# Optimization experiments

Hardware: AMD Instinct MI355X
Metric: run time of the kernel (lower is better)

The kernel has to match this reference:

```python
import jax, jax.numpy as jnp
import numpy as np

NUM_CATS = 8
ACTION_DIM = 64
HIDDEN = 1024  # out_type.size == config.hidden_size
N_TOKENS = 4096  # B*T
N_BATCH = 128    # timesteps batch; tiled to N_TOKENS in forward


def sinusoidal_pos_encoding(t, dim):
    # standard transformer sinusoidal encoding; t: (N,) -> (N, dim)
    half = dim // 2
    div = jnp.exp(jnp.arange(half, dtype=jnp.float32) * (-np.log(10000.0) / half))
    ang = t.astype(jnp.float32)[:, None] * div[None, :]          # (N, half)
    pe = jnp.stack([jnp.sin(ang), jnp.cos(ang)], axis=-1)        # (N, half, 2)
    return pe.reshape(t.shape[0], dim)


def cat_linear(x, W, b, cat_ids):
    """Per-category linear (gather -> per-group GEMM -> scatter-back, fused).
    x: (N, din), W: (C, din, dout), b: (C, dout), cat_ids: (N,) int.
    Mathematically identical to the torch loop over unique cat ids."""
    y_all = jnp.einsum('nd,cdo->nco', x, W)                      # dense dispatch over C
    y = jnp.take_along_axis(y_all, cat_ids[:, None, None], axis=1)[:, 0, :]
    return y + b[cat_ids]


def setup_inputs() -> dict:
    key = jax.random.key(0)
    ks = jax.random.split(key, 9)
    inp = {
        'actions': jax.random.normal(ks[0], (N_TOKENS, ACTION_DIM), dtype=jnp.float32),
        'timesteps': jax.random.randint(ks[1], (N_BATCH,), 0, 1000, dtype=jnp.int32),
        'cat_ids': jax.random.randint(ks[2], (N_TOKENS,), 0, NUM_CATS, dtype=jnp.int32),
        'W1': jax.random.normal(ks[3], (NUM_CATS, ACTION_DIM, HIDDEN), dtype=jnp.float32) / np.sqrt(ACTION_DIM),
        'b1': jax.random.normal(ks[4], (NUM_CATS, HIDDEN), dtype=jnp.float32) * 0.02,
        'W2': jax.random.normal(ks[5], (NUM_CATS, 2 * HIDDEN, HIDDEN), dtype=jnp.float32) / np.sqrt(2 * HIDDEN),
        'b2': jax.random.normal(ks[6], (NUM_CATS, HIDDEN), dtype=jnp.float32) * 0.02,
        'W3': jax.random.normal(ks[7], (NUM_CATS, HIDDEN, HIDDEN), dtype=jnp.float32) / np.sqrt(HIDDEN),
        'b3': jax.random.normal(ks[8], (NUM_CATS, HIDDEN), dtype=jnp.float32) * 0.02,
    }
    return inp


def reference(actions, timesteps, cat_ids, W1, b1, W2, b2, W3, b3):
    n = actions.shape[0]
    # timesteps.repeat(B // timesteps.shape[0]) in torch tiles the whole tensor
    t_full = jnp.tile(timesteps, n // timesteps.shape[0])        # (N,)
    a_emb = cat_linear(actions, W1, b1, cat_ids)                 # (N, H)
    tau_emb = sinusoidal_pos_encoding(t_full, HIDDEN).astype(a_emb.dtype)
    x = jnp.concatenate([a_emb, tau_emb], axis=-1)               # (N, 2H)
    x = jax.nn.silu(cat_linear(x, W2, b2, cat_ids))              # swish
    x = cat_linear(x, W3, b3, cat_ids)                           # (N, H)
    return x
```

## Files before the change

kernel.cpp:

```cpp
#include <hip/hip_runtime.h>
#include <cmath>


#define NTOK 4096
#define HID  1024
#define NC   8
#define MPAD 4224

typedef _Float16 f16;
typedef _Float16 f16x8 __attribute__((ext_vector_type(8)));
typedef float    f32x4 __attribute__((ext_vector_type(4)));

#define GLDS16(g, l) __builtin_amdgcn_global_load_lds(                      \
    (const __attribute__((address_space(1))) void*)(g),                     \
    (__attribute__((address_space(3))) void*)(l), 16, 0, 0)

__global__ void build_perm_kernel(const int* __restrict__ cat,
                                  int* __restrict__ perm,
                                  int* __restrict__ cat_off) {
  __shared__ int cnt[NC];
  __shared__ int off[NC + 1];
  const int tid = threadIdx.x;
  if (tid < NC) cnt[tid] = 0;
  __syncthreads();
  for (int n = tid; n < NTOK; n += blockDim.x) atomicAdd(&cnt[cat[n]], 1);
  __syncthreads();
  if (tid == 0) {
    int s = 0;
    for (int c = 0; c < NC; ++c) { off[c] = s; s += cnt[c]; }
    off[NC] = s;
  }
  __syncthreads();
  if (tid < NC) cnt[tid] = off[tid];
  if (tid <= NC) cat_off[tid] = off[tid];
  __syncthreads();
  for (int n = tid; n < NTOK; n += blockDim.x) {
    int pos = atomicAdd(&cnt[cat[n]], 1);
    perm[pos] = n;
  }
}

__global__ void tau16_kernel(const int* __restrict__ ts, f16* __restrict__ tau) {
  const int b = blockIdx.x;
  const float t = (float)ts[b];
  const float cdiv = -0.017988946039015984f;
  for (int i = threadIdx.x; i < HID / 2; i += blockDim.x) {
    float ang = t * expf(cdiv * (float)i);
    tau[(size_t)b * HID + 2 * i]     = (f16)sinf(ang);
    tau[(size_t)b * HID + 2 * i + 1] = (f16)cosf(ang);
  }
}

__global__ void gather_kernel(const float* __restrict__ actions,
                              const f16* __restrict__ tau,
                              const int* __restrict__ perm,
                              f16* __restrict__ act_g, f16* __restrict__ xcat) {
  const int r = blockIdx.x;
  const int tok = perm[r];
  const int t = threadIdx.x;
  if (t < 64) act_g[(size_t)r * 64 + t] = (f16)actions[(size_t)tok * 64 + t];
  const uint4* src = (const uint4*)(tau + (size_t)(tok & 127) * HID);
  uint4* dst = (uint4*)(xcat + (size_t)r * 2048 + HID);
  dst[t] = src[t];
}

__global__ __launch_bounds__(256) void wcvt_kernel(const float* __restrict__ W,
                                                   f16* __restrict__ Wt, int K) {
  const int c = blockIdx.z, k0 = blockIdx.y * 64, n0 = blockIdx.x * 64;
  __shared__ f16 tl[64][68];
  const int tid = threadIdx.x;
  const int rr = tid >> 4, cs = (tid & 15) * 4;
  const float* src = W + ((size_t)c * K + k0) * HID + n0;
#pragma unroll
  for (int it = 0; it < 4; ++it) {
    const int kr = rr + it * 16;
    float4 v = *(const float4*)(src + (size_t)kr * HID + cs);
    tl[kr][cs + 0] = (f16)v.x;
    tl[kr][cs + 1] = (f16)v.y;
    tl[kr][cs + 2] = (f16)v.z;
    tl[kr][cs + 3] = (f16)v.w;
  }
  __syncthreads();
  f16* dst = Wt + ((size_t)c * HID + n0) * K + k0;
#pragma unroll
  for (int it = 0; it < 4; ++it) {
    const int nr = rr + it * 16;
    union { f16 h[4]; uint2 u; } pk;
    pk.h[0] = tl[cs + 0][nr];
    pk.h[1] = tl[cs + 1][nr];
    pk.h[2] = tl[cs + 2][nr];
    pk.h[3] = tl[cs + 3][nr];
    *(uint2*)(dst + (size_t)nr * K + cs) = pk.u;
  }
}

template <int K, int MODE>
__global__ __launch_bounds__(512) void mfma_gemm(
    const f16* __restrict__ A, const f16* __restrict__ Wt,
    const float* __restrict__ Bias, const int* __restrict__ perm,
    const int* __restrict__ cat_off, void* __restrict__ OutV) {
  constexpr int PA = (MODE == 0) ? 64 : (MODE == 1) ? 2048 : 1024;
  constexpr int NT = K / 32;
  const int c = blockIdx.z;
  const int g0 = cat_off[c], cnt = cat_off[c + 1] - g0;
  const int m0 = blockIdx.y * 128;
  if (m0 >= cnt) return;
  const int n0 = blockIdx.x * 128;

  __shared__ f16 As[2][4096];
  __shared__ f16 Bs[2][4096];
  __shared__ int rows[128];

  const int tid = threadIdx.x;
  const int lane = tid & 63, wid = tid >> 6;

  if (MODE == 2 && tid < 128) {
    int m = m0 + tid;
    if (m > cnt - 1) m = cnt - 1;
    rows[tid] = perm[g0 + m];
  }

  const f16* Abase = A + (size_t)(g0 + m0) * PA;
  const f16* Bbase = Wt + ((size_t)c * HID + n0) * K;
  const int srow = tid >> 2, sks = (tid & 3) * 8;

  f32x4 acc[2][4];
#pragma unroll
  for (int i = 0; i < 2; ++i)
#pragma unroll
    for (int j = 0; j < 4; ++j) acc[i][j] = (f32x4){0.f, 0.f, 0.f, 0.f};

  const int wm = wid >> 1, wn = wid & 1;
  const int fr = lane & 15, fk = (lane >> 4) * 8;

#define STAGE(buf, kt)                                                \
  do {                                                                \
    GLDS16(Abase + (size_t)srow * PA + (kt) + sks, &As[buf][tid * 8]); \
    GLDS16(Bbase + (size_t)srow * K + (kt) + sks, &Bs[buf][tid * 8]);  \
  } while (0)

  STAGE(0, 0);
  __syncthreads();
  int cur = 0;
  for (int t = 0; t < NT; ++t) {
    if (t + 1 < NT) STAGE(cur ^ 1, (t + 1) * 32);
    f16x8 a[2], b[4];
#pragma unroll
    for (int i = 0; i < 2; ++i)
      a[i] = *(const f16x8*)&As[cur][(wm * 32 + i * 16 + fr) * 32 + fk];
#pragma unroll
    for (int j = 0; j < 4; ++j)
      b[j] = *(const f16x8*)&Bs[cur][(wn * 64 + j * 16 + fr) * 32 + fk];
#pragma unroll
    for (int i = 0; i < 2; ++i)
#pragma unroll
      for (int j = 0; j < 4; ++j)
        acc[i][j] = __builtin_amdgcn_mfma_f32_16x16x32_f16(a[i], b[j], acc[i][j], 0, 0, 0);
    __syncthreads();
    cur ^= 1;
  }
#undef STAGE

#pragma unroll
  for (int i = 0; i < 2; ++i) {
    const int mlbase = wm * 32 + i * 16 + (lane >> 4) * 4;
#pragma unroll
    for (int j = 0; j < 4; ++j) {
      const int col = wn * 64 + j * 16 + fr;
      const float bb = Bias[c * HID + n0 + col];
#pragma unroll
      for (int q = 0; q < 4; ++q) {
        const int ml = mlbase + q;
        if (m0 + ml >= cnt) continue;
        float v = acc[i][j][q] + bb;
        if (MODE == 1) v = v / (1.0f + __expf(-v));
        if (MODE == 2) {
          ((float*)OutV)[(size_t)rows[ml] * HID + n0 + col] = v;
        } else if (MODE == 1) {
          ((f16*)OutV)[(size_t)(g0 + m0 + ml) * HID + n0 + col] = (f16)v;
        } else {
          ((f16*)OutV)[(size_t)(g0 + m0 + ml) * 2048 + n0 + col] = (f16)v;
        }
      }
    }
  }
}

extern "C" void kernel_launch(void* const* d_in, const int* in_sizes, int n_in,
                              void* d_out, int out_size, void* d_ws, size_t ws_size,
                              hipStream_t stream) {
  const float* actions   = (const float*)d_in[0];
  const int*   timesteps = (const int*)d_in[1];
  const int*   cat_ids   = (const int*)d_in[2];
  const float* W1 = (const float*)d_in[3];
  const float* b1 = (const float*)d_in[4];
  const float* W2 = (const float*)d_in[5];
  const float* b2 = (const float*)d_in[6];
  const float* W3 = (const float*)d_in[7];
  const float* b3 = (const float*)d_in[8];
  float* out = (float*)d_out;

  char* ws = (char*)d_ws;
  const size_t MiB = 1u << 20;
  int* perm    = (int*)(ws + 0);
  int* cat_off = (int*)(ws + (16u << 10));
  f16* tau16   = (f16*)(ws + (32u << 10));
  f16* act_g   = (f16*)(ws + (512u << 10));
  f16* Wt1     = (f16*)(ws + 2 * MiB);
  f16* xcat    = (f16*)(ws + 3 * MiB);
  f16* h       = (f16*)(ws + 20 * MiB);
  f16* Wt2     = (f16*)(ws + 29 * MiB);
  f16* Wt3     = (f16*)(ws + 61 * MiB);

  build_perm_kernel<<<1, 256, 0, stream>>>(cat_ids, perm, cat_off);
  tau16_kernel<<<128, 256, 0, stream>>>(timesteps, tau16);
  gather_kernel<<<NTOK, 128, 0, stream>>>(actions, tau16, perm, act_g, xcat);

  wcvt_kernel<<<dim3(HID / 64, 1, NC), 256, 0, stream>>>(W1, Wt1, 64);
  wcvt_kernel<<<dim3(HID / 64, 32, NC), 256, 0, stream>>>(W2, Wt2, 2048);
  wcvt_kernel<<<dim3(HID / 64, 16, NC), 256, 0, stream>>>(W3, Wt3, 1024);

  dim3 ggrid(HID / 128, NTOK / 128, NC);
  mfma_gemm<64, 0><<<ggrid, 512, 0, stream>>>(act_g, Wt1, b1, perm, cat_off, xcat);
  mfma_gemm<2048, 1><<<ggrid, 512, 0, stream>>>(xcat, Wt2, b2, perm, cat_off, h);
  mfma_gemm<1024, 2><<<ggrid, 512, 0, stream>>>(h, Wt3, b3, perm, cat_off, out);
}
```

Before: 279.3 us.

## Compact tile map, 64-row tiles, BK=64 triple-buffered swizzled LDS pipeline

Builds a compact list of (category, row-offset) tiles in the permutation kernel so the GEMM grid only launches populated 64-row tiles instead of a sparse 3D grid with early exits. The GEMM moves to 256 threads with 64x128 tiles, a K-step of 64, three LDS buffers with explicit vmcnt waits and one barrier per step, and an XOR-swizzled LDS layout to reduce bank conflicts. The aim is better load balance, deeper prefetch and less LDS conflict and barrier overhead. The cost is more LDS per block and smaller M tiles, which reuse each weight tile across fewer rows.

```diff
diff --git a/kernel.cpp b/kernel.cpp
--- a/kernel.cpp
+++ b/kernel.cpp
@@ -14,10 +14,12 @@
 #define GLDS16(g, l) __builtin_amdgcn_global_load_lds(                      \
     (const __attribute__((address_space(1))) void*)(g),                     \
     (__attribute__((address_space(3))) void*)(l), 16, 0, 0)
+#define WAITV(n) asm volatile("s_waitcnt vmcnt(" #n ")" ::: "memory")
 
 __global__ void build_perm_kernel(const int* __restrict__ cat,
                                   int* __restrict__ perm,
-                                  int* __restrict__ cat_off) {
+                                  int* __restrict__ cat_off,
+                                  int* __restrict__ tmap) {
   __shared__ int cnt[NC];
   __shared__ int off[NC + 1];
   const int tid = threadIdx.x;
@@ -29,6 +31,12 @@
     int s = 0;
     for (int c = 0; c < NC; ++c) { off[c] = s; s += cnt[c]; }
     off[NC] = s;
+    int ns = 0;
+    for (int c = 0; c < NC; ++c) {
+      const int n = off[c + 1] - off[c];
+      for (int m0 = 0; m0 < n; m0 += 64) tmap[1 + ns++] = (c << 20) | m0;
+    }
+    tmap[0] = ns;
   }
   __syncthreads();
   if (tid < NC) cnt[tid] = off[tid];
@@ -95,26 +103,32 @@
 }
 
 template <int K, int MODE>
-__global__ __launch_bounds__(512) void mfma_gemm(
+__global__ __launch_bounds__(256, 2) void mfma_gemm(
     const f16* __restrict__ A, const f16* __restrict__ Wt,
     const float* __restrict__ Bias, const int* __restrict__ perm,
-    const int* __restrict__ cat_off, void* __restrict__ OutV) {
+    const int* __restrict__ cat_off, const int* __restrict__ tmap,
+    void* __restrict__ OutV) {
   constexpr int PA = (MODE == 0) ? 64 : (MODE == 1) ? 2048 : 1024;
-  constexpr int NT = K / 32;
-  const int c = blockIdx.z;
+  constexpr int BK = 64;
+  constexpr int NT = K / BK;
+
+  const int nslots = tmap[0];
+  if ((int)blockIdx.y >= nslots) return;
+  const int ent = tmap[1 + blockIdx.y];
+  const int c = ent >> 20, m0 = ent & 0xFFF;
   const int g0 = cat_off[c], cnt = cat_off[c + 1] - g0;
-  const int m0 = blockIdx.y * 128;
-  if (m0 >= cnt) return;
   const int n0 = blockIdx.x * 128;
 
-  __shared__ f16 As[2][4096];
-  __shared__ f16 Bs[2][4096];
-  __shared__ int rows[128];
+  __shared__ f16 As[3][64 * BK];
+  __shared__ f16 Bs[3][128 * BK];
+  __shared__ int rows[64];
 
   const int tid = threadIdx.x;
   const int lane = tid & 63, wid = tid >> 6;
-
-  if (MODE == 2 && tid < 128) {
+  const int wm = wid >> 1, wn = wid & 1;
+  const int fr = lane & 15, fq = lane >> 4;
+
+  if (MODE == 2 && tid < 64) {
     int m = m0 + tid;
     if (m > cnt - 1) m = cnt - 1;
     rows[tid] = perm[g0 + m];
@@ -122,7 +136,20 @@
 
   const f16* Abase = A + (size_t)(g0 + m0) * PA;
   const f16* Bbase = Wt + ((size_t)c * HID + n0) * K;
-  const int srow = tid >> 2, sks = (tid & 3) * 8;
+
+#define STAGE(buf, kt)                                                        \
+  do {                                                                        \
+    _Pragma("unroll") for (int i_ = 0; i_ < 2; ++i_) {                        \
+      const int s_ = tid + i_ * 256;                                          \
+      const int r_ = s_ >> 3, qg_ = (s_ & 7) ^ (r_ & 7);                      \
+      GLDS16(Abase + (size_t)r_ * PA + (kt) + qg_ * 8, &As[buf][s_ * 8]);     \
+    }                                                                         \
+    _Pragma("unroll") for (int i_ = 0; i_ < 4; ++i_) {                        \
+      const int s_ = tid + i_ * 256;                                          \
+      const int r_ = s_ >> 3, qg_ = (s_ & 7) ^ (r_ & 7);                      \
+      GLDS16(Bbase + (size_t)r_ * K + (kt) + qg_ * 8, &Bs[buf][s_ * 8]);      \
+    }                                                                         \
+  } while (0)
 
   f32x4 acc[2][4];
 #pragma unroll
@@ -130,47 +157,51 @@
 #pragma unroll
     for (int j = 0; j < 4; ++j) acc[i][j] = (f32x4){0.f, 0.f, 0.f, 0.f};
 
-  const int wm = wid >> 1, wn = wid & 1;
-  const int fr = lane & 15, fk = (lane >> 4) * 8;
-
-#define STAGE(buf, kt)                                                \
-  do {                                                                \
-    GLDS16(Abase + (size_t)srow * PA + (kt) + sks, &As[buf][tid * 8]); \
-    GLDS16(Bbase + (size_t)srow * K + (kt) + sks, &Bs[buf][tid * 8]);  \
-  } while (0)
-
   STAGE(0, 0);
-  __syncthreads();
-  int cur = 0;
+  if (NT > 1) STAGE(1, BK);
+
   for (int t = 0; t < NT; ++t) {
-    if (t + 1 < NT) STAGE(cur ^ 1, (t + 1) * 32);
-    f16x8 a[2], b[4];
-#pragma unroll
-    for (int i = 0; i < 2; ++i)
-      a[i] = *(const f16x8*)&As[cur][(wm * 32 + i * 16 + fr) * 32 + fk];
-#pragma unroll
-    for (int j = 0; j < 4; ++j)
-      b[j] = *(const f16x8*)&Bs[cur][(wn * 64 + j * 16 + fr) * 32 + fk];
-#pragma unroll
-    for (int i = 0; i < 2; ++i)
-#pragma unroll
-      for (int j = 0; j < 4; ++j)
-        acc[i][j] = __builtin_amdgcn_mfma_f32_16x16x32_f16(a[i], b[j], acc[i][j], 0, 0, 0);
-    __syncthreads();
-    cur ^= 1;
+    if (t + 1 < NT) { WAITV(6); } else { WAITV(0); }
+    __builtin_amdgcn_s_barrier();
+    const int cur = t % 3;
+
+    f16x8 af[2][2], bf[2][4];
+#pragma unroll
+    for (int ks = 0; ks < 2; ++ks) {
+      const int q = ks * 4 + fq;
+#pragma unroll
+      for (int i = 0; i < 2; ++i) {
+        const int r = wm * 32 + i * 16 + fr;
+        af[ks][i] = *(const f16x8*)&As[cur][r * 64 + ((q ^ (r & 7)) * 8)];
+      }
+#pragma unroll
+      for (int j = 0; j < 4; ++j) {
+        const int r = wn * 64 + j * 16 + fr;
+        bf[ks][j] = *(const f16x8*)&Bs[cur][r * 64 + ((q ^ (r & 7)) * 8)];
+      }
+    }
+#pragma unroll
+    for (int ks = 0; ks < 2; ++ks)
+#pragma unroll
+      for (int i = 0; i < 2; ++i)
+#pragma unroll
+        for (int j = 0; j < 4; ++j)
+          acc[i][j] = __builtin_amdgcn_mfma_f32_16x16x32_f16(af[ks][i], bf[ks][j],
+                                                             acc[i][j], 0, 0, 0);
+    if (t + 2 < NT) STAGE((t + 2) % 3, (t + 2) * BK);
   }
 #undef STAGE
 
 #pragma unroll
   for (int i = 0; i < 2; ++i) {
-    const int mlbase = wm * 32 + i * 16 + (lane >> 4) * 4;
+    const int mlb = wm * 32 + i * 16 + fq * 4;
 #pragma unroll
     for (int j = 0; j < 4; ++j) {
       const int col = wn * 64 + j * 16 + fr;
       const float bb = Bias[c * HID + n0 + col];
 #pragma unroll
       for (int q = 0; q < 4; ++q) {
-        const int ml = mlbase + q;
+        const int ml = mlb + q;
         if (m0 + ml >= cnt) continue;
         float v = acc[i][j][q] + bb;
         if (MODE == 1) v = v / (1.0f + __expf(-v));
@@ -204,6 +235,7 @@
   const size_t MiB = 1u << 20;
   int* perm    = (int*)(ws + 0);
   int* cat_off = (int*)(ws + (16u << 10));
+  int* tmap    = (int*)(ws + (20u << 10));
   f16* tau16   = (f16*)(ws + (32u << 10));
   f16* act_g   = (f16*)(ws + (512u << 10));
   f16* Wt1     = (f16*)(ws + 2 * MiB);
@@ -212,7 +244,7 @@
   f16* Wt2     = (f16*)(ws + 29 * MiB);
   f16* Wt3     = (f16*)(ws + 61 * MiB);
 
-  build_perm_kernel<<<1, 256, 0, stream>>>(cat_ids, perm, cat_off);
+  build_perm_kernel<<<1, 256, 0, stream>>>(cat_ids, perm, cat_off, tmap);
   tau16_kernel<<<128, 256, 0, stream>>>(timesteps, tau16);
   gather_kernel<<<NTOK, 128, 0, stream>>>(actions, tau16, perm, act_g, xcat);
 
@@ -220,8 +252,8 @@
   wcvt_kernel<<<dim3(HID / 64, 32, NC), 256, 0, stream>>>(W2, Wt2, 2048);
   wcvt_kernel<<<dim3(HID / 64, 16, NC), 256, 0, stream>>>(W3, Wt3, 1024);
 
-  dim3 ggrid(HID / 128, NTOK / 128, NC);
-  mfma_gemm<64, 0><<<ggrid, 512, 0, stream>>>(act_g, Wt1, b1, perm, cat_off, xcat);
-  mfma_gemm<2048, 1><<<ggrid, 512, 0, stream>>>(xcat, Wt2, b2, perm, cat_off, h);
-  mfma_gemm<1024, 2><<<ggrid, 512, 0, stream>>>(h, Wt3, b3, perm, cat_off, out);
-}
+  dim3 ggrid(HID / 128, 72, 1);
+  mfma_gemm<64, 0><<<ggrid, 256, 0, stream>>>(act_g, Wt1, b1, perm, cat_off, tmap, xcat);
+  mfma_gemm<2048, 1><<<ggrid, 256, 0, stream>>>(xcat, Wt2, b2, perm, cat_off, tmap, h);
+  mfma_gemm<1024, 2><<<ggrid, 256, 0, stream>>>(h, Wt3, b3, perm, cat_off, tmap, out);
+}
```

Result: faster. 262.0 us (-6.2%).
